# Performance work log

Measured on AMD Instinct MI355X. Metric: run time of the kernel, lower is better.

## Reference

```python
import jax, jax.numpy as jnp
import numpy as np

N = 1000   # node count forced by fc1_1 in_features=1680 (see shape derivation)
E = 8000   # edges, avg degree ~8
F_IN = 6   # node feature dim (first 3 = pos, zeroed in forward)


def setup_inputs() -> dict:
    key = jax.random.key(0)
    ks = jax.random.split(key, 24)
    f = lambda k, s, sc=1.0: jax.random.normal(k, s, dtype=jnp.float32) * sc
    inp = {
        "x": f(ks[0], (N, F_IN)),
        "edge_index": jax.random.randint(ks[1], (2, E), 0, N, dtype=jnp.int64),
        # GCNConv weights (xavier-ish scale)
        "W1": f(ks[2], (F_IN, 32), 0.4), "b1": jnp.zeros((32,), jnp.float32),
        "W2": f(ks[3], (32, 32), 0.18), "b2": jnp.zeros((32,), jnp.float32),
        # Conv2d kernels, OIHW
        "k1": f(ks[4], (3, 1, 3, 2), 0.3), "kb1": jnp.zeros((3,), jnp.float32),
        "k2": f(ks[5], (6, 3, 3, 2), 0.2), "kb2": jnp.zeros((6,), jnp.float32),
        "k3": f(ks[6], (3, 6, 3, 2), 0.2), "kb3": jnp.zeros((3,), jnp.float32),
        "k4": f(ks[7], (1, 3, 3, 2), 0.2), "kb4": jnp.zeros((1,), jnp.float32),
        # FC head (torch Linear layout: [out, in])
        "fw1": f(ks[8], (1024, 1680), 0.02), "fb1": jnp.zeros((1024,), jnp.float32),
        "fw2": f(ks[9], (1024, 1024), 0.03), "fb2": jnp.zeros((1024,), jnp.float32),
        "fw3": f(ks[10], (64, 1024), 0.03), "fb3": jnp.zeros((64,), jnp.float32),
    }
    return inp


def _conv2d(x, w, b):
    out = jax.lax.conv_general_dilated(
        x, w, window_strides=(1, 1), padding="VALID",
        dimension_numbers=("NCHW", "OIHW", "NCHW"))
    return out + b[None, :, None, None]


def _maxpool2(x):  # MaxPool2d((2,1), stride=(2,1))
    return jax.lax.reduce_window(x, -jnp.inf, jax.lax.max,
                                 (1, 1, 2, 1), (1, 1, 2, 1), "VALID")


def reference(x, edge_index, W1, b1, W2, b2, k1, kb1, k2, kb2, k3, kb3, k4, kb4,
              fw1, fb1, fw2, fb2, fw3, fb3):
    num_nodes = x.shape[0]
    # forward zeroes the first 3 features (positions)
    x = x.at[:, :3].set(0.0)

    loop = jnp.arange(num_nodes)
    row = jnp.concatenate([edge_index[0], loop])
    col = jnp.concatenate([edge_index[1], loop])
    deg = jnp.zeros((num_nodes,), x.dtype).at[col].add(1.0)
    dinv = jnp.where(deg > 0, jax.lax.rsqrt(deg), 0.0)
    norm = (dinv[row] * dinv[col])[:, None]  # [E+N, 1]

    def gcn(h, W, b):
        hw = h @ W                                   # [N, 32]
        msg = hw[row] * norm                         # gather + scale
        return jax.ops.segment_sum(msg, col, num_segments=num_nodes) + b

    leaky = lambda v: jnp.where(v > 0, v, 0.2 * v)   # LeakyReLU(0.2)
    h = leaky(gcn(x, W1, b1))
    h = leaky(gcn(h, W2, b2))                        # [N, 32]

    img = h[None, None]                              # [1, 1, N, 32]
    img = _maxpool2(jax.nn.relu(_conv2d(img, k1, kb1)))   # [1,3,499,31]
    img = _maxpool2(jax.nn.relu(_conv2d(img, k2, kb2)))   # [1,6,248,30]
    img = _maxpool2(jax.nn.relu(_conv2d(img, k3, kb3)))   # [1,3,123,29]
    img = _maxpool2(jax.nn.relu(_conv2d(img, k4, kb4)))   # [1,1,60,28]

    v = img.reshape(-1)                              # [1680]
    v = v @ fw1.T + fb1                              # no activation between FCs (as in source)
    v = v @ fw2.T + fb2
    v = v @ fw3.T + fb3                              # [64]
    return v
```

## Files before the change

kernel.cpp:

```cpp
#include <hip/hip_runtime.h>

#define LEAKY(v) ((v) > 0.0f ? (v) : 0.2f * (v))

__global__ void k_init(float* __restrict__ deg, float* __restrict__ agg1,
                       float* __restrict__ agg2, int n, int aggn) {
    int tid = blockIdx.x * blockDim.x + threadIdx.x;
    if (tid < n) deg[tid] = 1.0f;
    if (tid < aggn) { agg1[tid] = 0.0f; agg2[tid] = 0.0f; }
}

__global__ void k_deg(const int* __restrict__ col, float* __restrict__ deg, int E) {
    int e = blockIdx.x * blockDim.x + threadIdx.x;
    if (e < E) atomicAdd(&deg[col[e]], 1.0f);
}

__global__ void k_xw1(const float* __restrict__ x, const float* __restrict__ W1,
                      float* __restrict__ xw, float* __restrict__ deg, int n) {
    int tid = blockIdx.x * blockDim.x + threadIdx.x;
    if (tid >= n * 32) return;
    int j = tid & 31, nn = tid >> 5;
    if (j == 0) deg[nn] = 1.0f / sqrtf(deg[nn]);
    xw[tid] = x[nn * 6 + 3] * W1[96 + j]
            + x[nn * 6 + 4] * W1[128 + j]
            + x[nn * 6 + 5] * W1[160 + j];
}

__global__ void k_scatter(const float* __restrict__ xw, const float* __restrict__ dinv,
                          const int* __restrict__ row, const int* __restrict__ col,
                          float* __restrict__ agg, int E, int n) {
    int tid = blockIdx.x * blockDim.x + threadIdx.x;
    int total = (E + n) * 32;
    if (tid >= total) return;
    int e = tid >> 5, j = tid & 31;
    int r, c; float nrm;
    if (e < E) { r = row[e]; c = col[e]; nrm = dinv[r] * dinv[c]; }
    else       { r = c = e - E; float d = dinv[r]; nrm = d * d; }
    atomicAdd(&agg[c * 32 + j], xw[r * 32 + j] * nrm);
}

__global__ void k_xw2(const float* __restrict__ agg1, const float* __restrict__ b1,
                      const float* __restrict__ W2, float* __restrict__ xw, int n) {
    int tid = blockIdx.x * blockDim.x + threadIdx.x;
    if (tid >= n * 32) return;
    int j = tid & 31, nn = tid >> 5;
    const float* a = agg1 + nn * 32;
    float s = 0.0f;
#pragma unroll
    for (int f = 0; f < 32; ++f) {
        float v = a[f] + b1[f];
        v = LEAKY(v);
        s += v * W2[f * 32 + j];
    }
    xw[tid] = s;
}

__global__ void k_conv1_pool(const float* __restrict__ h2, const float* __restrict__ b2,
                             const float* __restrict__ w, const float* __restrict__ bias,
                             float* __restrict__ out, int Hp, int Wo) {
    int tid = blockIdx.x * blockDim.x + threadIdx.x;
    int total = 3 * Hp * Wo;
    if (tid >= total) return;
    int ow = tid % Wo; int t = tid / Wo; int oh = t % Hp; int co = t / Hp;
    const float* ip = h2 + (2 * oh) * 32 + ow;
    float vals[4][2];
#pragma unroll
    for (int r = 0; r < 4; ++r)
#pragma unroll
        for (int cx = 0; cx < 2; ++cx) {
            float v = ip[r * 32 + cx] + b2[ow + cx];
            vals[r][cx] = LEAKY(v);
        }
    const float* wp = w + co * 6;
    float acc0 = vals[0][0]*wp[0] + vals[0][1]*wp[1] + vals[1][0]*wp[2]
               + vals[1][1]*wp[3] + vals[2][0]*wp[4] + vals[2][1]*wp[5];
    float acc1 = vals[1][0]*wp[0] + vals[1][1]*wp[1] + vals[2][0]*wp[2]
               + vals[2][1]*wp[3] + vals[3][0]*wp[4] + vals[3][1]*wp[5];
    float m = fmaxf(acc0, acc1) + bias[co];
    out[tid] = fmaxf(m, 0.0f);
}

__global__ void k_conv_pool(const float* __restrict__ in, const float* __restrict__ w,
                            const float* __restrict__ bias, float* __restrict__ out,
                            int CI, int CO, int Hin, int Win, int Hp, int Wo) {
    int tid = blockIdx.x * blockDim.x + threadIdx.x;
    int total = CO * Hp * Wo;
    if (tid >= total) return;
    int ow = tid % Wo; int t = tid / Wo; int oh = t % Hp; int co = t / Hp;
    float acc0 = 0.0f, acc1 = 0.0f;
    for (int ci = 0; ci < CI; ++ci) {
        const float* ip = in + (ci * Hin + 2 * oh) * Win + ow;
        const float* wp = w + (co * CI + ci) * 6;
        float r00 = ip[0],         r01 = ip[1];
        float r10 = ip[Win],       r11 = ip[Win + 1];
        float r20 = ip[2 * Win],   r21 = ip[2 * Win + 1];
        float r30 = ip[3 * Win],   r31 = ip[3 * Win + 1];
        acc0 += r00*wp[0] + r01*wp[1] + r10*wp[2] + r11*wp[3] + r20*wp[4] + r21*wp[5];
        acc1 += r10*wp[0] + r11*wp[1] + r20*wp[2] + r21*wp[3] + r30*wp[4] + r31*wp[5];
    }
    float m = fmaxf(acc0, acc1) + bias[co];
    out[tid] = fmaxf(m, 0.0f);
}

template <int BLOCK>
__global__ void k_fc(const float* __restrict__ v, const float* __restrict__ w,
                     const float* __restrict__ b, float* __restrict__ out, int IN) {
    int o = blockIdx.x;
    const float* wr = w + (size_t)o * IN;
    float s = 0.0f;
    for (int i = threadIdx.x; i < IN; i += BLOCK) s += v[i] * wr[i];
#pragma unroll
    for (int off = 32; off > 0; off >>= 1) s += __shfl_down(s, off, 64);
    __shared__ float ls[BLOCK / 64];
    int lane = threadIdx.x & 63, wv = threadIdx.x >> 6;
    if (lane == 0) ls[wv] = s;
    __syncthreads();
    if (threadIdx.x == 0) {
        float t = 0.0f;
#pragma unroll
        for (int i = 0; i < BLOCK / 64; ++i) t += ls[i];
        out[o] = t + b[o];
    }
}

extern "C" void kernel_launch(void* const* d_in, const int* in_sizes, int n_in,
                              void* d_out, int out_size, void* d_ws, size_t ws_size,
                              hipStream_t stream) {
    const float* x   = (const float*)d_in[0];
    const int*   ei  = (const int*)d_in[1];
    const float* W1  = (const float*)d_in[2];
    const float* b1  = (const float*)d_in[3];
    const float* W2  = (const float*)d_in[4];
    const float* b2  = (const float*)d_in[5];
    const float* k1  = (const float*)d_in[6];
    const float* kb1 = (const float*)d_in[7];
    const float* k2  = (const float*)d_in[8];
    const float* kb2 = (const float*)d_in[9];
    const float* k3  = (const float*)d_in[10];
    const float* kb3 = (const float*)d_in[11];
    const float* k4  = (const float*)d_in[12];
    const float* kb4 = (const float*)d_in[13];
    const float* fw1 = (const float*)d_in[14];
    const float* fb1 = (const float*)d_in[15];
    const float* fw2 = (const float*)d_in[16];
    const float* fb2 = (const float*)d_in[17];
    const float* fw3 = (const float*)d_in[18];
    const float* fb3 = (const float*)d_in[19];

    int n = in_sizes[0] / 6;
    int E = in_sizes[1] / 2;
    const int* row = ei;
    const int* col = ei + E;

    float* ws   = (float*)d_ws;
    float* deg  = ws;
    float* xw   = ws + 1024;
    float* agg1 = xw + n * 32;
    float* agg2 = agg1 + n * 32;

    int H1 = (n - 2) / 2,  W1o = 31;
    int H2 = (H1 - 2) / 2, W2o = 30;
    int H3 = (H2 - 2) / 2, W3o = 29;
    int H4 = (H3 - 2) / 2, W4o = 28;
    float* c1 = agg2 + n * 32;
    float* c2 = c1 + 3 * H1 * W1o;
    float* c3 = c2 + 6 * H2 * W2o;
    float* c4 = c3 + 3 * H3 * W3o;
    float* f1 = c4 + H4 * W4o;
    float* f2 = f1 + 1024;

    const int B = 256;
    int aggn = n * 32;
    int initn = (aggn > n) ? aggn : n;

    k_init<<<(initn + B - 1) / B, B, 0, stream>>>(deg, agg1, agg2, n, aggn);
    k_deg<<<(E + B - 1) / B, B, 0, stream>>>(col, deg, E);
    k_xw1<<<(n * 32 + B - 1) / B, B, 0, stream>>>(x, W1, xw, deg, n);
    int st = (E + n) * 32;
    k_scatter<<<(st + B - 1) / B, B, 0, stream>>>(xw, deg, row, col, agg1, E, n);
    k_xw2<<<(n * 32 + B - 1) / B, B, 0, stream>>>(agg1, b1, W2, xw, n);
    k_scatter<<<(st + B - 1) / B, B, 0, stream>>>(xw, deg, row, col, agg2, E, n);

    k_conv1_pool<<<(3 * H1 * W1o + B - 1) / B, B, 0, stream>>>(agg2, b2, k1, kb1, c1, H1, W1o);
    k_conv_pool<<<(6 * H2 * W2o + B - 1) / B, B, 0, stream>>>(c1, k2, kb2, c2, 3, 6, H1, W1o, H2, W2o);
    k_conv_pool<<<(3 * H3 * W3o + B - 1) / B, B, 0, stream>>>(c2, k3, kb3, c3, 6, 3, H2, W2o, H3, W3o);
    k_conv_pool<<<(1 * H4 * W4o + B - 1) / B, B, 0, stream>>>(c3, k4, kb4, c4, 3, 1, H3, W3o, H4, W4o);

    int IN1 = H4 * W4o;
    k_fc<256><<<1024, 256, 0, stream>>>(c4, fw1, fb1, f1, IN1);
    k_fc<256><<<1024, 256, 0, stream>>>(f1, fw2, fb2, f2, 1024);
    k_fc<256><<<64, 256, 0, stream>>>(f2, fw3, fb3, (float*)d_out, 1024);
}
```

Before: 136.8 us.

## Fuse entire GCN-CNN-FC pipeline into one cooperative persistent kernel with grid syncs

```diff
diff --git a/kernel.cpp b/kernel.cpp
--- a/kernel.cpp
+++ b/kernel.cpp
@@ -1,192 +1,242 @@
 #include <hip/hip_runtime.h>
+#include <hip/hip_cooperative_groups.h>
+
+namespace cg = cooperative_groups;
 
 #define LEAKY(v) ((v) > 0.0f ? (v) : 0.2f * (v))
 
-__global__ void k_init(float* __restrict__ deg, float* __restrict__ agg1,
-                       float* __restrict__ agg2, int n, int aggn) {
-    int tid = blockIdx.x * blockDim.x + threadIdx.x;
-    if (tid < n) deg[tid] = 1.0f;
-    if (tid < aggn) { agg1[tid] = 0.0f; agg2[tid] = 0.0f; }
+struct P {
+    const float* x; const int* row; const int* col;
+    const float* W1; const float* b1; const float* W2; const float* b2;
+    const float* k1; const float* kb1; const float* k2; const float* kb2;
+    const float* k3; const float* kb3; const float* k4; const float* kb4;
+    const float* fw1; const float* fb1; const float* fw2; const float* fb2;
+    const float* fw3; const float* fb3;
+    float* deg; float* agg1; float* agg2; float* xw;
+    float* c1; float* c2; float* c3; float* f1; float* f2; float* out;
+    int n; int E;
+};
+
+__device__ inline void scatter_stage(const P& p, const float* __restrict__ xw,
+                                     float* __restrict__ agg, int tid, int NT) {
+    int total = (p.E + p.n) * 32;
+    for (int t = tid; t < total; t += NT) {
+        int e = t >> 5, j = t & 31;
+        int r, c;
+        if (e < p.E) { r = p.row[e]; c = p.col[e]; }
+        else         { r = c = e - p.E; }
+        float nrm = (1.0f / sqrtf(p.deg[r])) * (1.0f / sqrtf(p.deg[c]));
+        atomicAdd(&agg[c * 32 + j], xw[r * 32 + j] * nrm);
+    }
 }
 
-__global__ void k_deg(const int* __restrict__ col, float* __restrict__ deg, int E) {
-    int e = blockIdx.x * blockDim.x + threadIdx.x;
-    if (e < E) atomicAdd(&deg[col[e]], 1.0f);
-}
-
-__global__ void k_xw1(const float* __restrict__ x, const float* __restrict__ W1,
-                      float* __restrict__ xw, float* __restrict__ deg, int n) {
-    int tid = blockIdx.x * blockDim.x + threadIdx.x;
-    if (tid >= n * 32) return;
-    int j = tid & 31, nn = tid >> 5;
-    if (j == 0) deg[nn] = 1.0f / sqrtf(deg[nn]);
-    xw[tid] = x[nn * 6 + 3] * W1[96 + j]
-            + x[nn * 6 + 4] * W1[128 + j]
-            + x[nn * 6 + 5] * W1[160 + j];
-}
-
-__global__ void k_scatter(const float* __restrict__ xw, const float* __restrict__ dinv,
-                          const int* __restrict__ row, const int* __restrict__ col,
-                          float* __restrict__ agg, int E, int n) {
-    int tid = blockIdx.x * blockDim.x + threadIdx.x;
-    int total = (E + n) * 32;
-    if (tid >= total) return;
-    int e = tid >> 5, j = tid & 31;
-    int r, c; float nrm;
-    if (e < E) { r = row[e]; c = col[e]; nrm = dinv[r] * dinv[c]; }
-    else       { r = c = e - E; float d = dinv[r]; nrm = d * d; }
-    atomicAdd(&agg[c * 32 + j], xw[r * 32 + j] * nrm);
-}
-
-__global__ void k_xw2(const float* __restrict__ agg1, const float* __restrict__ b1,
-                      const float* __restrict__ W2, float* __restrict__ xw, int n) {
-    int tid = blockIdx.x * blockDim.x + threadIdx.x;
-    if (tid >= n * 32) return;
-    int j = tid & 31, nn = tid >> 5;
-    const float* a = agg1 + nn * 32;
-    float s = 0.0f;
-#pragma unroll
-    for (int f = 0; f < 32; ++f) {
-        float v = a[f] + b1[f];
-        v = LEAKY(v);
-        s += v * W2[f * 32 + j];
-    }
-    xw[tid] = s;
-}
-
-__global__ void k_conv1_pool(const float* __restrict__ h2, const float* __restrict__ b2,
-                             const float* __restrict__ w, const float* __restrict__ bias,
-                             float* __restrict__ out, int Hp, int Wo) {
-    int tid = blockIdx.x * blockDim.x + threadIdx.x;
-    int total = 3 * Hp * Wo;
-    if (tid >= total) return;
-    int ow = tid % Wo; int t = tid / Wo; int oh = t % Hp; int co = t / Hp;
-    const float* ip = h2 + (2 * oh) * 32 + ow;
-    float vals[4][2];
-#pragma unroll
-    for (int r = 0; r < 4; ++r)
-#pragma unroll
-        for (int cx = 0; cx < 2; ++cx) {
-            float v = ip[r * 32 + cx] + b2[ow + cx];
-            vals[r][cx] = LEAKY(v);
-        }
-    const float* wp = w + co * 6;
-    float acc0 = vals[0][0]*wp[0] + vals[0][1]*wp[1] + vals[1][0]*wp[2]
-               + vals[1][1]*wp[3] + vals[2][0]*wp[4] + vals[2][1]*wp[5];
-    float acc1 = vals[1][0]*wp[0] + vals[1][1]*wp[1] + vals[2][0]*wp[2]
-               + vals[2][1]*wp[3] + vals[3][0]*wp[4] + vals[3][1]*wp[5];
-    float m = fmaxf(acc0, acc1) + bias[co];
-    out[tid] = fmaxf(m, 0.0f);
-}
-
-__global__ void k_conv_pool(const float* __restrict__ in, const float* __restrict__ w,
-                            const float* __restrict__ bias, float* __restrict__ out,
-                            int CI, int CO, int Hin, int Win, int Hp, int Wo) {
-    int tid = blockIdx.x * blockDim.x + threadIdx.x;
-    int total = CO * Hp * Wo;
-    if (tid >= total) return;
-    int ow = tid % Wo; int t = tid / Wo; int oh = t % Hp; int co = t / Hp;
-    float acc0 = 0.0f, acc1 = 0.0f;
-    for (int ci = 0; ci < CI; ++ci) {
-        const float* ip = in + (ci * Hin + 2 * oh) * Win + ow;
-        const float* wp = w + (co * CI + ci) * 6;
-        float r00 = ip[0],         r01 = ip[1];
-        float r10 = ip[Win],       r11 = ip[Win + 1];
-        float r20 = ip[2 * Win],   r21 = ip[2 * Win + 1];
-        float r30 = ip[3 * Win],   r31 = ip[3 * Win + 1];
-        acc0 += r00*wp[0] + r01*wp[1] + r10*wp[2] + r11*wp[3] + r20*wp[4] + r21*wp[5];
-        acc1 += r10*wp[0] + r11*wp[1] + r20*wp[2] + r21*wp[3] + r30*wp[4] + r31*wp[5];
-    }
-    float m = fmaxf(acc0, acc1) + bias[co];
-    out[tid] = fmaxf(m, 0.0f);
-}
-
-template <int BLOCK>
-__global__ void k_fc(const float* __restrict__ v, const float* __restrict__ w,
-                     const float* __restrict__ b, float* __restrict__ out, int IN) {
-    int o = blockIdx.x;
-    const float* wr = w + (size_t)o * IN;
-    float s = 0.0f;
-    for (int i = threadIdx.x; i < IN; i += BLOCK) s += v[i] * wr[i];
-#pragma unroll
-    for (int off = 32; off > 0; off >>= 1) s += __shfl_down(s, off, 64);
-    __shared__ float ls[BLOCK / 64];
-    int lane = threadIdx.x & 63, wv = threadIdx.x >> 6;
-    if (lane == 0) ls[wv] = s;
-    __syncthreads();
-    if (threadIdx.x == 0) {
-        float t = 0.0f;
-#pragma unroll
-        for (int i = 0; i < BLOCK / 64; ++i) t += ls[i];
-        out[o] = t + b[o];
+__global__ __launch_bounds__(256, 1) void k_all(P p) {
+    cg::grid_group grid = cg::this_grid();
+    const int tid = blockIdx.x * blockDim.x + threadIdx.x;
+    const int NT  = gridDim.x * blockDim.x;
+    const int n = p.n, E = p.E;
+
+    for (int i = tid; i < n + E; i += NT) {
+        int c = (i < n) ? i : p.col[i - n];
+        atomicAdd(&p.deg[c], 1.0f);
+    }
+    for (int t = tid; t < n * 32; t += NT) {
+        int j = t & 31, nn = t >> 5;
+        p.xw[t] = p.x[nn*6+3] * p.W1[96+j]
+                + p.x[nn*6+4] * p.W1[128+j]
+                + p.x[nn*6+5] * p.W1[160+j];
+    }
+    grid.sync();
+
+    scatter_stage(p, p.xw, p.agg1, tid, NT);
+    grid.sync();
+
+    for (int t = tid; t < n * 32; t += NT) {
+        int j = t & 31, nn = t >> 5;
+        const float* a = p.agg1 + nn * 32;
+        float s = 0.0f;
+#pragma unroll
+        for (int f = 0; f < 32; ++f) {
+            float v = a[f] + p.b1[f];
+            v = LEAKY(v);
+            s += v * p.W2[f * 32 + j];
+        }
+        p.xw[t] = s;
+    }
+    grid.sync();
+
+    scatter_stage(p, p.xw, p.agg2, tid, NT);
+    grid.sync();
+
+    {
+        const int Hp = 499, Wo = 31, total = 3 * Hp * Wo;
+        for (int t0 = tid; t0 < total; t0 += NT) {
+            int ow = t0 % Wo; int t = t0 / Wo; int oh = t % Hp; int co = t / Hp;
+            const float* ip = p.agg2 + (2 * oh) * 32 + ow;
+            float vals[4][2];
+#pragma unroll
+            for (int r = 0; r < 4; ++r)
+#pragma unroll
+                for (int cx = 0; cx < 2; ++cx) {
+                    float v = ip[r * 32 + cx] + p.b2[ow + cx];
+                    vals[r][cx] = LEAKY(v);
+                }
+            const float* wp = p.k1 + co * 6;
+            float a0 = vals[0][0]*wp[0] + vals[0][1]*wp[1] + vals[1][0]*wp[2]
+                     + vals[1][1]*wp[3] + vals[2][0]*wp[4] + vals[2][1]*wp[5];
+            float a1 = vals[1][0]*wp[0] + vals[1][1]*wp[1] + vals[2][0]*wp[2]
+                     + vals[2][1]*wp[3] + vals[3][0]*wp[4] + vals[3][1]*wp[5];
+            float m = fmaxf(a0, a1) + p.kb1[co];
+            p.c1[t0] = fmaxf(m, 0.0f);
+        }
+    }
+    grid.sync();
+
+    {
+        const int CI = 3, Hin = 499, Win = 31, Hp = 248, Wo = 30, total = 6 * Hp * Wo;
+        for (int t0 = tid; t0 < total; t0 += NT) {
+            int ow = t0 % Wo; int t = t0 / Wo; int oh = t % Hp; int co = t / Hp;
+            float a0 = 0.0f, a1 = 0.0f;
+            for (int ci = 0; ci < CI; ++ci) {
+                const float* ip = p.c1 + (ci * Hin + 2 * oh) * Win + ow;
+                const float* wp = p.k2 + (co * CI + ci) * 6;
+                float r00 = ip[0],       r01 = ip[1];
+                float r10 = ip[Win],     r11 = ip[Win+1];
+                float r20 = ip[2*Win],   r21 = ip[2*Win+1];
+                float r30 = ip[3*Win],   r31 = ip[3*Win+1];
+                a0 += r00*wp[0] + r01*wp[1] + r10*wp[2] + r11*wp[3] + r20*wp[4] + r21*wp[5];
+                a1 += r10*wp[0] + r11*wp[1] + r20*wp[2] + r21*wp[3] + r30*wp[4] + r31*wp[5];
+            }
+            float m = fmaxf(a0, a1) + p.kb2[co];
+            p.c2[t0] = fmaxf(m, 0.0f);
+        }
+    }
+    grid.sync();
+
+    {
+        const int CI = 6, Hin = 248, Win = 30, Hp = 123, Wo = 29, total = 3 * Hp * Wo;
+        for (int t0 = tid; t0 < total; t0 += NT) {
+            int ow = t0 % Wo; int t = t0 / Wo; int oh = t % Hp; int co = t / Hp;
+            float a0 = 0.0f, a1 = 0.0f;
+            for (int ci = 0; ci < CI; ++ci) {
+                const float* ip = p.c3 , *dummy = ip; (void)dummy;
+                const float* q = p.c2 + (ci * Hin + 2 * oh) * Win + ow;
+                const float* wp = p.k3 + (co * CI + ci) * 6;
+                float r00 = q[0],       r01 = q[1];
+                float r10 = q[Win],     r11 = q[Win+1];
+                float r20 = q[2*Win],   r21 = q[2*Win+1];
+                float r30 = q[3*Win],   r31 = q[3*Win+1];
+                a0 += r00*wp[0] + r01*wp[1] + r10*wp[2] + r11*wp[3] + r20*wp[4] + r21*wp[5];
+                a1 += r10*wp[0] + r11*wp[1] + r20*wp[2] + r21*wp[3] + r30*wp[4] + r31*wp[5];
+            }
+            float m = fmaxf(a0, a1) + p.kb3[co];
+            p.c3[t0] = fmaxf(m, 0.0f);
+        }
+    }
+    grid.sync();
+
+    __shared__ float lc4[1680];
+    {
+        const int CI = 3, Hin = 123, Win = 29, Wo = 28;
+        for (int t0 = (int)threadIdx.x; t0 < 1680; t0 += (int)blockDim.x) {
+            int ow = t0 % Wo; int oh = t0 / Wo;
+            float a0 = 0.0f, a1 = 0.0f;
+            for (int ci = 0; ci < CI; ++ci) {
+                const float* q = p.c3 + (ci * Hin + 2 * oh) * Win + ow;
+                const float* wp = p.k4 + ci * 6;
+                float r00 = q[0],       r01 = q[1];
+                float r10 = q[Win],     r11 = q[Win+1];
+                float r20 = q[2*Win],   r21 = q[2*Win+1];
+                float r30 = q[3*Win],   r31 = q[3*Win+1];
+                a0 += r00*wp[0] + r01*wp[1] + r10*wp[2] + r11*wp[3] + r20*wp[4] + r21*wp[5];
+                a1 += r10*wp[0] + r11*wp[1] + r20*wp[2] + r21*wp[3] + r30*wp[4] + r31*wp[5];
+            }
+            float m = fmaxf(a0, a1) + p.kb4[0];
+            lc4[t0] = fmaxf(m, 0.0f);
+        }
+        __syncthreads();
+        int wv = threadIdx.x >> 6, lane = threadIdx.x & 63;
+        int o = blockIdx.x * 4 + wv;
+        const float* wr = p.fw1 + (size_t)o * 1680;
+        float s = 0.0f;
+        for (int i = lane; i < 1680; i += 64) s += lc4[i] * wr[i];
+#pragma unroll
+        for (int off = 32; off > 0; off >>= 1) s += __shfl_down(s, off, 64);
+        if (lane == 0) p.f1[o] = s + p.fb1[o];
+    }
+    grid.sync();
+
+    {
+        int wv = threadIdx.x >> 6, lane = threadIdx.x & 63;
+        int o = blockIdx.x * 4 + wv;
+        const float* wr = p.fw2 + (size_t)o * 1024;
+        float s = 0.0f;
+        for (int i = lane; i < 1024; i += 64) s += p.f1[i] * wr[i];
+#pragma unroll
+        for (int off = 32; off > 0; off >>= 1) s += __shfl_down(s, off, 64);
+        if (lane == 0) p.f2[o] = s + p.fb2[o];
+    }
+    grid.sync();
+
+    {
+        int wv = threadIdx.x >> 6, lane = threadIdx.x & 63;
+        int o = blockIdx.x * 4 + wv;
+        if (o < 64) {
+            const float* wr = p.fw3 + (size_t)o * 1024;
+            float s = 0.0f;
+            for (int i = lane; i < 1024; i += 64) s += p.f2[i] * wr[i];
+#pragma unroll
+            for (int off = 32; off > 0; off >>= 1) s += __shfl_down(s, off, 64);
+            if (lane == 0) p.out[o] = s + p.fb3[o];
+        }
     }
 }
 
 extern "C" void kernel_launch(void* const* d_in, const int* in_sizes, int n_in,
                               void* d_out, int out_size, void* d_ws, size_t ws_size,
                               hipStream_t stream) {
-    const float* x   = (const float*)d_in[0];
-    const int*   ei  = (const int*)d_in[1];
-    const float* W1  = (const float*)d_in[2];
-    const float* b1  = (const float*)d_in[3];
-    const float* W2  = (const float*)d_in[4];
-    const float* b2  = (const float*)d_in[5];
-    const float* k1  = (const float*)d_in[6];
-    const float* kb1 = (const float*)d_in[7];
-    const float* k2  = (const float*)d_in[8];
-    const float* kb2 = (const float*)d_in[9];
-    const float* k3  = (const float*)d_in[10];
-    const float* kb3 = (const float*)d_in[11];
-    const float* k4  = (const float*)d_in[12];
-    const float* kb4 = (const float*)d_in[13];
-    const float* fw1 = (const float*)d_in[14];
-    const float* fb1 = (const float*)d_in[15];
-    const float* fw2 = (const float*)d_in[16];
-    const float* fb2 = (const float*)d_in[17];
-    const float* fw3 = (const float*)d_in[18];
-    const float* fb3 = (const float*)d_in[19];
-
-    int n = in_sizes[0] / 6;
-    int E = in_sizes[1] / 2;
-    const int* row = ei;
-    const int* col = ei + E;
-
-    float* ws   = (float*)d_ws;
-    float* deg  = ws;
-    float* xw   = ws + 1024;
-    float* agg1 = xw + n * 32;
-    float* agg2 = agg1 + n * 32;
-
-    int H1 = (n - 2) / 2,  W1o = 31;
-    int H2 = (H1 - 2) / 2, W2o = 30;
-    int H3 = (H2 - 2) / 2, W3o = 29;
-    int H4 = (H3 - 2) / 2, W4o = 28;
-    float* c1 = agg2 + n * 32;
-    float* c2 = c1 + 3 * H1 * W1o;
-    float* c3 = c2 + 6 * H2 * W2o;
-    float* c4 = c3 + 3 * H3 * W3o;
-    float* f1 = c4 + H4 * W4o;
-    float* f2 = f1 + 1024;
-
-    const int B = 256;
-    int aggn = n * 32;
-    int initn = (aggn > n) ? aggn : n;
-
-    k_init<<<(initn + B - 1) / B, B, 0, stream>>>(deg, agg1, agg2, n, aggn);
-    k_deg<<<(E + B - 1) / B, B, 0, stream>>>(col, deg, E);
-    k_xw1<<<(n * 32 + B - 1) / B, B, 0, stream>>>(x, W1, xw, deg, n);
-    int st = (E + n) * 32;
-    k_scatter<<<(st + B - 1) / B, B, 0, stream>>>(xw, deg, row, col, agg1, E, n);
-    k_xw2<<<(n * 32 + B - 1) / B, B, 0, stream>>>(agg1, b1, W2, xw, n);
-    k_scatter<<<(st + B - 1) / B, B, 0, stream>>>(xw, deg, row, col, agg2, E, n);
-
-    k_conv1_pool<<<(3 * H1 * W1o + B - 1) / B, B, 0, stream>>>(agg2, b2, k1, kb1, c1, H1, W1o);
-    k_conv_pool<<<(6 * H2 * W2o + B - 1) / B, B, 0, stream>>>(c1, k2, kb2, c2, 3, 6, H1, W1o, H2, W2o);
-    k_conv_pool<<<(3 * H3 * W3o + B - 1) / B, B, 0, stream>>>(c2, k3, kb3, c3, 6, 3, H2, W2o, H3, W3o);
-    k_conv_pool<<<(1 * H4 * W4o + B - 1) / B, B, 0, stream>>>(c3, k4, kb4, c4, 3, 1, H3, W3o, H4, W4o);
-
-    int IN1 = H4 * W4o;
-    k_fc<256><<<1024, 256, 0, stream>>>(c4, fw1, fb1, f1, IN1);
-    k_fc<256><<<1024, 256, 0, stream>>>(f1, fw2, fb2, f2, 1024);
-    k_fc<256><<<64, 256, 0, stream>>>(f2, fw3, fb3, (float*)d_out, 1024);
+    P p;
+    p.x   = (const float*)d_in[0];
+    const int* ei = (const int*)d_in[1];
+    p.W1  = (const float*)d_in[2];
+    p.b1  = (const float*)d_in[3];
+    p.W2  = (const float*)d_in[4];
+    p.b2  = (const float*)d_in[5];
+    p.k1  = (const float*)d_in[6];
+    p.kb1 = (const float*)d_in[7];
+    p.k2  = (const float*)d_in[8];
+    p.kb2 = (const float*)d_in[9];
+    p.k3  = (const float*)d_in[10];
+    p.kb3 = (const float*)d_in[11];
+    p.k4  = (const float*)d_in[12];
+    p.kb4 = (const float*)d_in[13];
+    p.fw1 = (const float*)d_in[14];
+    p.fb1 = (const float*)d_in[15];
+    p.fw2 = (const float*)d_in[16];
+    p.fb2 = (const float*)d_in[17];
+    p.fw3 = (const float*)d_in[18];
+    p.fb3 = (const float*)d_in[19];
+
+    p.n = in_sizes[0] / 6;
+    p.E = in_sizes[1] / 2;
+    p.row = ei;
+    p.col = ei + p.E;
+
+    float* ws = (float*)d_ws;
+    p.deg  = ws;
+    p.agg1 = ws + 1024;
+    p.agg2 = p.agg1 + 32000;
+    p.xw   = p.agg2 + 32000;
+    p.c1   = p.xw + 32000;
+    p.c2   = p.c1 + 46407;
+    p.c3   = p.c2 + 44640;
+    p.f1   = p.c3 + 10701;
+    p.f2   = p.f1 + 1024;
+    p.out  = (float*)d_out;
+
+    hipMemsetAsync(d_ws, 0, (1024 + 64000) * sizeof(float), stream);
+
+    void* args[] = { &p };
+    hipLaunchCooperativeKernel((const void*)k_all, dim3(256), dim3(256),
+                               args, 0, stream);
 }
```

New measurement: 404.8 us. +196.0%, slower.

## Fuse GCN prep kernels, conv3/conv4 into FC1, and use one wave per FC row

Applied to the files above, without the earlier changes.

```diff
diff --git a/kernel.cpp b/kernel.cpp
--- a/kernel.cpp
+++ b/kernel.cpp
@@ -2,30 +2,23 @@
 
 #define LEAKY(v) ((v) > 0.0f ? (v) : 0.2f * (v))
 
-__global__ void k_init(float* __restrict__ deg, float* __restrict__ agg1,
-                       float* __restrict__ agg2, int n, int aggn) {
+__global__ void k1_prep(const float* __restrict__ x, const int* __restrict__ col,
+                        const float* __restrict__ W1, float* __restrict__ deg,
+                        float* __restrict__ aggs ,
+                        float* __restrict__ xw, int n, int E) {
     int tid = blockIdx.x * blockDim.x + threadIdx.x;
-    if (tid < n) deg[tid] = 1.0f;
-    if (tid < aggn) { agg1[tid] = 0.0f; agg2[tid] = 0.0f; }
-}
-
-__global__ void k_deg(const int* __restrict__ col, float* __restrict__ deg, int E) {
-    int e = blockIdx.x * blockDim.x + threadIdx.x;
-    if (e < E) atomicAdd(&deg[col[e]], 1.0f);
-}
-
-__global__ void k_xw1(const float* __restrict__ x, const float* __restrict__ W1,
-                      float* __restrict__ xw, float* __restrict__ deg, int n) {
-    int tid = blockIdx.x * blockDim.x + threadIdx.x;
-    if (tid >= n * 32) return;
-    int j = tid & 31, nn = tid >> 5;
-    if (j == 0) deg[nn] = 1.0f / sqrtf(deg[nn]);
-    xw[tid] = x[nn * 6 + 3] * W1[96 + j]
-            + x[nn * 6 + 4] * W1[128 + j]
-            + x[nn * 6 + 5] * W1[160 + j];
-}
-
-__global__ void k_scatter(const float* __restrict__ xw, const float* __restrict__ dinv,
+    int NT = gridDim.x * blockDim.x;
+    for (int i = tid; i < 2 * n * 32; i += NT) aggs[i] = 0.0f;
+    for (int e = tid; e < E; e += NT) atomicAdd(&deg[col[e]], 1.0f);
+    for (int t = tid; t < n * 32; t += NT) {
+        int j = t & 31, nn = t >> 5;
+        xw[t] = x[nn*6+3] * W1[96+j]
+              + x[nn*6+4] * W1[128+j]
+              + x[nn*6+5] * W1[160+j];
+    }
+}
+
+__global__ void k_scatter(const float* __restrict__ xw, const float* __restrict__ deg,
                           const int* __restrict__ row, const int* __restrict__ col,
                           float* __restrict__ agg, int E, int n) {
     int tid = blockIdx.x * blockDim.x + threadIdx.x;
@@ -33,13 +26,18 @@
     if (tid >= total) return;
     int e = tid >> 5, j = tid & 31;
     int r, c; float nrm;
-    if (e < E) { r = row[e]; c = col[e]; nrm = dinv[r] * dinv[c]; }
-    else       { r = c = e - E; float d = dinv[r]; nrm = d * d; }
+    if (e < E) {
+        r = row[e]; c = col[e];
+        nrm = (1.0f / sqrtf(deg[r] + 1.0f)) * (1.0f / sqrtf(deg[c] + 1.0f));
+    } else {
+        r = c = e - E;
+        nrm = 1.0f / (deg[r] + 1.0f);
+    }
     atomicAdd(&agg[c * 32 + j], xw[r * 32 + j] * nrm);
 }
 
-__global__ void k_xw2(const float* __restrict__ agg1, const float* __restrict__ b1,
-                      const float* __restrict__ W2, float* __restrict__ xw, int n) {
+__global__ void k3_xw2(const float* __restrict__ agg1, const float* __restrict__ b1,
+                       const float* __restrict__ W2, float* __restrict__ xw, int n) {
     int tid = blockIdx.x * blockDim.x + threadIdx.x;
     if (tid >= n * 32) return;
     int j = tid & 31, nn = tid >> 5;
@@ -54,13 +52,13 @@
     xw[tid] = s;
 }
 
-__global__ void k_conv1_pool(const float* __restrict__ h2, const float* __restrict__ b2,
-                             const float* __restrict__ w, const float* __restrict__ bias,
-                             float* __restrict__ out, int Hp, int Wo) {
-    int tid = blockIdx.x * blockDim.x + threadIdx.x;
-    int total = 3 * Hp * Wo;
-    if (tid >= total) return;
-    int ow = tid % Wo; int t = tid / Wo; int oh = t % Hp; int co = t / Hp;
+__global__ void k5_conv1(const float* __restrict__ h2, const float* __restrict__ b2,
+                         const float* __restrict__ w, const float* __restrict__ bias,
+                         float* __restrict__ out) {
+    const int Hp = 499, Wo = 31, total = 3 * Hp * Wo;
+    int t0 = blockIdx.x * blockDim.x + threadIdx.x;
+    if (t0 >= total) return;
+    int ow = t0 % Wo; int t = t0 / Wo; int oh = t % Hp; int co = t / Hp;
     const float* ip = h2 + (2 * oh) * 32 + ow;
     float vals[4][2];
 #pragma unroll
@@ -71,55 +69,107 @@
             vals[r][cx] = LEAKY(v);
         }
     const float* wp = w + co * 6;
-    float acc0 = vals[0][0]*wp[0] + vals[0][1]*wp[1] + vals[1][0]*wp[2]
-               + vals[1][1]*wp[3] + vals[2][0]*wp[4] + vals[2][1]*wp[5];
-    float acc1 = vals[1][0]*wp[0] + vals[1][1]*wp[1] + vals[2][0]*wp[2]
-               + vals[2][1]*wp[3] + vals[3][0]*wp[4] + vals[3][1]*wp[5];
-    float m = fmaxf(acc0, acc1) + bias[co];
-    out[tid] = fmaxf(m, 0.0f);
-}
-
-__global__ void k_conv_pool(const float* __restrict__ in, const float* __restrict__ w,
-                            const float* __restrict__ bias, float* __restrict__ out,
-                            int CI, int CO, int Hin, int Win, int Hp, int Wo) {
-    int tid = blockIdx.x * blockDim.x + threadIdx.x;
-    int total = CO * Hp * Wo;
-    if (tid >= total) return;
-    int ow = tid % Wo; int t = tid / Wo; int oh = t % Hp; int co = t / Hp;
-    float acc0 = 0.0f, acc1 = 0.0f;
+    float a0 = vals[0][0]*wp[0] + vals[0][1]*wp[1] + vals[1][0]*wp[2]
+             + vals[1][1]*wp[3] + vals[2][0]*wp[4] + vals[2][1]*wp[5];
+    float a1 = vals[1][0]*wp[0] + vals[1][1]*wp[1] + vals[2][0]*wp[2]
+             + vals[2][1]*wp[3] + vals[3][0]*wp[4] + vals[3][1]*wp[5];
+    float m = fmaxf(a0, a1) + bias[co];
+    out[t0] = fmaxf(m, 0.0f);
+}
+
+__global__ void k6_conv2(const float* __restrict__ in, const float* __restrict__ w,
+                         const float* __restrict__ bias, float* __restrict__ out) {
+    const int CI = 3, Hin = 499, Win = 31, Hp = 248, Wo = 30, total = 6 * Hp * Wo;
+    int t0 = blockIdx.x * blockDim.x + threadIdx.x;
+    if (t0 >= total) return;
+    int ow = t0 % Wo; int t = t0 / Wo; int oh = t % Hp; int co = t / Hp;
+    float a0 = 0.0f, a1 = 0.0f;
+#pragma unroll
     for (int ci = 0; ci < CI; ++ci) {
-        const float* ip = in + (ci * Hin + 2 * oh) * Win + ow;
+        const float* q = in + (ci * Hin + 2 * oh) * Win + ow;
         const float* wp = w + (co * CI + ci) * 6;
-        float r00 = ip[0],         r01 = ip[1];
-        float r10 = ip[Win],       r11 = ip[Win + 1];
-        float r20 = ip[2 * Win],   r21 = ip[2 * Win + 1];
-        float r30 = ip[3 * Win],   r31 = ip[3 * Win + 1];
-        acc0 += r00*wp[0] + r01*wp[1] + r10*wp[2] + r11*wp[3] + r20*wp[4] + r21*wp[5];
-        acc1 += r10*wp[0] + r11*wp[1] + r20*wp[2] + r21*wp[3] + r30*wp[4] + r31*wp[5];
-    }
-    float m = fmaxf(acc0, acc1) + bias[co];
-    out[tid] = fmaxf(m, 0.0f);
-}
-
-template <int BLOCK>
-__global__ void k_fc(const float* __restrict__ v, const float* __restrict__ w,
-                     const float* __restrict__ b, float* __restrict__ out, int IN) {
-    int o = blockIdx.x;
+        float r00 = q[0],     r01 = q[1];
+        float r10 = q[Win],   r11 = q[Win+1];
+        float r20 = q[2*Win], r21 = q[2*Win+1];
+        float r30 = q[3*Win], r31 = q[3*Win+1];
+        a0 += r00*wp[0] + r01*wp[1] + r10*wp[2] + r11*wp[3] + r20*wp[4] + r21*wp[5];
+        a1 += r10*wp[0] + r11*wp[1] + r20*wp[2] + r21*wp[3] + r30*wp[4] + r31*wp[5];
+    }
+    float m = fmaxf(a0, a1) + bias[co];
+    out[t0] = fmaxf(m, 0.0f);
+}
+
+__global__ __launch_bounds__(256) void k7_conv34_fc1(
+        const float* __restrict__ c2, const float* __restrict__ k3,
+        const float* __restrict__ kb3, const float* __restrict__ k4,
+        const float* __restrict__ kb4, const float* __restrict__ fw1,
+        const float* __restrict__ fb1, float* __restrict__ f1) {
+    __shared__ float lc3[3 * 123 * 29];
+    __shared__ float lc4[1680];
+    {
+        const int CI = 6, Hin = 248, Win = 30, Hp = 123, Wo = 29, total = 3 * Hp * Wo;
+        for (int t0 = (int)threadIdx.x; t0 < total; t0 += 256) {
+            int ow = t0 % Wo; int t = t0 / Wo; int oh = t % Hp; int co = t / Hp;
+            float a0 = 0.0f, a1 = 0.0f;
+#pragma unroll
+            for (int ci = 0; ci < CI; ++ci) {
+                const float* q = c2 + (ci * Hin + 2 * oh) * Win + ow;
+                const float* wp = k3 + (co * CI + ci) * 6;
+                float r00 = q[0],     r01 = q[1];
+                float r10 = q[Win],   r11 = q[Win+1];
+                float r20 = q[2*Win], r21 = q[2*Win+1];
+                float r30 = q[3*Win], r31 = q[3*Win+1];
+                a0 += r00*wp[0] + r01*wp[1] + r10*wp[2] + r11*wp[3] + r20*wp[4] + r21*wp[5];
+                a1 += r10*wp[0] + r11*wp[1] + r20*wp[2] + r21*wp[3] + r30*wp[4] + r31*wp[5];
+            }
+            float m = fmaxf(a0, a1) + kb3[co];
+            lc3[t0] = fmaxf(m, 0.0f);
+        }
+    }
+    __syncthreads();
+    {
+        const int CI = 3, Hin = 123, Win = 29, Wo = 28;
+        for (int t0 = (int)threadIdx.x; t0 < 1680; t0 += 256) {
+            int ow = t0 % Wo; int oh = t0 / Wo;
+            float a0 = 0.0f, a1 = 0.0f;
+#pragma unroll
+            for (int ci = 0; ci < CI; ++ci) {
+                const float* q = lc3 + (ci * Hin + 2 * oh) * Win + ow;
+                const float* wp = k4 + ci * 6;
+                float r00 = q[0],     r01 = q[1];
+                float r10 = q[Win],   r11 = q[Win+1];
+                float r20 = q[2*Win], r21 = q[2*Win+1];
+                float r30 = q[3*Win], r31 = q[3*Win+1];
+                a0 += r00*wp[0] + r01*wp[1] + r10*wp[2] + r11*wp[3] + r20*wp[4] + r21*wp[5];
+                a1 += r10*wp[0] + r11*wp[1] + r20*wp[2] + r21*wp[3] + r30*wp[4] + r31*wp[5];
+            }
+            float m = fmaxf(a0, a1) + kb4[0];
+            lc4[t0] = fmaxf(m, 0.0f);
+        }
+    }
+    __syncthreads();
+    int wv = threadIdx.x >> 6, lane = threadIdx.x & 63;
+    int o = blockIdx.x * 4 + wv;
+    const float* wr = fw1 + (size_t)o * 1680;
+    float s = 0.0f;
+    for (int i = lane; i < 1680; i += 64) s += lc4[i] * wr[i];
+#pragma unroll
+    for (int off = 32; off > 0; off >>= 1) s += __shfl_down(s, off, 64);
+    if (lane == 0) f1[o] = s + fb1[o];
+}
+
+__global__ __launch_bounds__(256) void k_fc(const float* __restrict__ v,
+                                            const float* __restrict__ w,
+                                            const float* __restrict__ b,
+                                            float* __restrict__ out, int IN) {
+    int wv = threadIdx.x >> 6, lane = threadIdx.x & 63;
+    int o = blockIdx.x * 4 + wv;
     const float* wr = w + (size_t)o * IN;
     float s = 0.0f;
-    for (int i = threadIdx.x; i < IN; i += BLOCK) s += v[i] * wr[i];
+    for (int i = lane; i < IN; i += 64) s += v[i] * wr[i];
 #pragma unroll
     for (int off = 32; off > 0; off >>= 1) s += __shfl_down(s, off, 64);
-    __shared__ float ls[BLOCK / 64];
-    int lane = threadIdx.x & 63, wv = threadIdx.x >> 6;
-    if (lane == 0) ls[wv] = s;
-    __syncthreads();
-    if (threadIdx.x == 0) {
-        float t = 0.0f;
-#pragma unroll
-        for (int i = 0; i < BLOCK / 64; ++i) t += ls[i];
-        out[o] = t + b[o];
-    }
+    if (lane == 0) out[o] = s + b[o];
 }
 
 extern "C" void kernel_launch(void* const* d_in, const int* in_sizes, int n_in,
@@ -153,40 +203,25 @@
 
     float* ws   = (float*)d_ws;
     float* deg  = ws;
-    float* xw   = ws + 1024;
-    float* agg1 = xw + n * 32;
-    float* agg2 = agg1 + n * 32;
-
-    int H1 = (n - 2) / 2,  W1o = 31;
-    int H2 = (H1 - 2) / 2, W2o = 30;
-    int H3 = (H2 - 2) / 2, W3o = 29;
-    int H4 = (H3 - 2) / 2, W4o = 28;
-    float* c1 = agg2 + n * 32;
-    float* c2 = c1 + 3 * H1 * W1o;
-    float* c3 = c2 + 6 * H2 * W2o;
-    float* c4 = c3 + 3 * H3 * W3o;
-    float* f1 = c4 + H4 * W4o;
-    float* f2 = f1 + 1024;
+    float* agg1 = ws + 1024;
+    float* agg2 = agg1 + 32000;
+    float* xw   = agg2 + 32000;
+    float* c1   = xw + 32000;
+    float* c2   = c1 + 46407;
+    float* f1   = c2 + 44640;
+    float* f2   = f1 + 1024;
 
     const int B = 256;
-    int aggn = n * 32;
-    int initn = (aggn > n) ? aggn : n;
-
-    k_init<<<(initn + B - 1) / B, B, 0, stream>>>(deg, agg1, agg2, n, aggn);
-    k_deg<<<(E + B - 1) / B, B, 0, stream>>>(col, deg, E);
-    k_xw1<<<(n * 32 + B - 1) / B, B, 0, stream>>>(x, W1, xw, deg, n);
+
+    hipMemsetAsync(deg, 0, n * sizeof(float), stream);
+    k1_prep<<<256, B, 0, stream>>>(x, col, W1, deg, agg1, xw, n, E);
     int st = (E + n) * 32;
     k_scatter<<<(st + B - 1) / B, B, 0, stream>>>(xw, deg, row, col, agg1, E, n);
-    k_xw2<<<(n * 32 + B - 1) / B, B, 0, stream>>>(agg1, b1, W2, xw, n);
+    k3_xw2<<<(n * 32 + B - 1) / B, B, 0, stream>>>(agg1, b1, W2, xw, n);
     k_scatter<<<(st + B - 1) / B, B, 0, stream>>>(xw, deg, row, col, agg2, E, n);
-
-    k_conv1_pool<<<(3 * H1 * W1o + B - 1) / B, B, 0, stream>>>(agg2, b2, k1, kb1, c1, H1, W1o);
-    k_conv_pool<<<(6 * H2 * W2o + B - 1) / B, B, 0, stream>>>(c1, k2, kb2, c2, 3, 6, H1, W1o, H2, W2o);
-    k_conv_pool<<<(3 * H3 * W3o + B - 1) / B, B, 0, stream>>>(c2, k3, kb3, c3, 6, 3, H2, W2o, H3, W3o);
-    k_conv_pool<<<(1 * H4 * W4o + B - 1) / B, B, 0, stream>>>(c3, k4, kb4, c4, 3, 1, H3, W3o, H4, W4o);
-
-    int IN1 = H4 * W4o;
-    k_fc<256><<<1024, 256, 0, stream>>>(c4, fw1, fb1, f1, IN1);
-    k_fc<256><<<1024, 256, 0, stream>>>(f1, fw2, fb2, f2, 1024);
-    k_fc<256><<<64, 256, 0, stream>>>(f2, fw3, fb3, (float*)d_out, 1024);
-}
+    k5_conv1<<<(3 * 499 * 31 + B - 1) / B, B, 0, stream>>>(agg2, b2, k1, kb1, c1);
+    k6_conv2<<<(6 * 248 * 30 + B - 1) / B, B, 0, stream>>>(c1, k2, kb2, c2);
+    k7_conv34_fc1<<<256, B, 0, stream>>>(c2, k3, kb3, k4, kb4, fw1, fb1, f1);
+    k_fc<<<256, B, 0, stream>>>(f1, fw2, fb2, f2, 1024);
+    k_fc<<<16, B, 0, stream>>>(f2, fw3, fb3, (float*)d_out, 1024);
+}
```

Result: slower. 234.6 us (+71.6%).
